# Kernel tuning notes

Measured on AMD Instinct MI355X. Metric: run time of the kernel, lower is better.

The kernel has to match this reference:

```python
import jax, jax.numpy as jnp
import numpy as np

D = 768
H = 16
DH = D // H  # 48
SCALE = 1.0 / np.sqrt(DH).astype(np.float32)
EPS = 1e-3  # keras LayerNormalization default epsilon
NEG = -1e9


def setup_inputs() -> dict:
    key = jax.random.key(0)
    ks = jax.random.split(key, 10)
    B, S = 4, 2048
    q = jax.random.normal(ks[0], (B, S, D), dtype=jnp.float32)
    k = jax.random.normal(ks[1], (B, S, D), dtype=jnp.float32)
    v = jax.random.normal(ks[2], (B, S, D), dtype=jnp.float32)
    # Dense projection params (glorot-ish scale)
    w_std = 1.0 / np.sqrt(D)
    Wq = jax.random.normal(ks[3], (D, D), dtype=jnp.float32) * w_std
    Wk = jax.random.normal(ks[4], (D, D), dtype=jnp.float32) * w_std
    Wv = jax.random.normal(ks[5], (D, D), dtype=jnp.float32) * w_std
    bq = jnp.zeros((D,), jnp.float32)
    bk = jnp.zeros((D,), jnp.float32)
    bv = jnp.zeros((D,), jnp.float32)
    gamma = jnp.ones((D,), jnp.float32)
    beta = jnp.zeros((D,), jnp.float32)
    return {"q": q, "k": k, "v": v, "Wq": Wq, "bq": bq, "Wk": Wk, "bk": bk,
            "Wv": Wv, "bv": bv, "gamma": gamma, "beta": beta}


def reference(q, k, v, Wq, bq, Wk, bk, Wv, bv, gamma, beta):
    use_causal = True  # exercise the causal-mask path
    B, S, _ = q.shape
    # Projections, then split into heads (tf.split on last axis == reshape)
    Q = (q @ Wq + bq).reshape(B, S, H, DH)
    K = (k @ Wk + bk).reshape(B, S, H, DH)
    V = (v @ Wv + bv).reshape(B, S, H, DH)
    # scores: [B, H, Sq, Sk]
    scores = jnp.einsum('bqhd,bkhd->bhqk', Q, K) * SCALE
    if use_causal:
        qi = jnp.arange(S)[:, None]
        ki = jnp.arange(S)[None, :]
        mask = jnp.where(qi >= ki, 0.0, NEG).astype(scores.dtype)
        scores = scores + mask
    attn = jax.nn.softmax(scores, axis=-1)
    out = jnp.einsum('bhqk,bkhd->bqhd', attn, V).reshape(B, S, D)
    # LayerNorm over last dim
    mu = jnp.mean(out, axis=-1, keepdims=True)
    var = jnp.mean(jnp.square(out - mu), axis=-1, keepdims=True)
    return (out - mu) * jax.lax.rsqrt(var + EPS) * gamma + beta
```

## Files before the change

kernel.cpp:

```cpp
#include <hip/hip_runtime.h>
#include <hip/hip_bf16.h>


#define DMODEL 768
#define NHEAD  16
#define DHEAD  48
#define SEQ    2048
#define NBATCH 4
#define NROWS  (NBATCH * SEQ)
#define QSCALE (0.14433756729740643f * 1.4426950408889634f)

typedef __bf16 bf16x8 __attribute__((ext_vector_type(8)));
typedef float  f32x4  __attribute__((ext_vector_type(4)));

#define GLDS16(g, l) __builtin_amdgcn_global_load_lds(                         \
    (const __attribute__((address_space(1))) unsigned int*)(g),                \
    (__attribute__((address_space(3))) unsigned int*)(l), 16, 0, 0)

__global__ __launch_bounds__(256) void transpose_w(
    const float* __restrict__ Wq,
    const float* __restrict__ Wk,
    const float* __restrict__ Wv,
    __hip_bfloat16* __restrict__ Wt)
{
    __shared__ __hip_bfloat16 tile[32][33];
    int bid = blockIdx.x;
    int mat = bid / 576;
    int t   = bid - mat * 576;
    int tr  = t / 24, tc = t - (t / 24) * 24;
    const float* W = (mat == 0) ? Wq : (mat == 1) ? Wk : Wv;
    __hip_bfloat16* O = Wt + (size_t)mat * DMODEL * DMODEL;
    int tx = threadIdx.x & 31, ty = threadIdx.x >> 5;
#pragma unroll
    for (int i = 0; i < 32; i += 8)
        tile[ty + i][tx] = __float2bfloat16(W[(size_t)(tr * 32 + ty + i) * DMODEL + tc * 32 + tx]);
    __syncthreads();
#pragma unroll
    for (int i = 0; i < 32; i += 8)
        O[(size_t)(tc * 32 + ty + i) * DMODEL + tr * 32 + tx] = tile[tx][ty + i];
}

__global__ __launch_bounds__(256) void qkv_proj(
    const float* __restrict__ xq,
    const float* __restrict__ xk,
    const float* __restrict__ xv,
    const __hip_bfloat16* __restrict__ Wt,
    const float* __restrict__ bq,
    const float* __restrict__ bk,
    const float* __restrict__ bv,
    __hip_bfloat16* __restrict__ Qr,
    __hip_bfloat16* __restrict__ Kr,
    __hip_bfloat16* __restrict__ Vt)
{
    __shared__ __hip_bfloat16 As[128 * 32];
    __shared__ __hip_bfloat16 Bs[128 * 32];

    int bid = blockIdx.x;
    int mat = bid / 384;
    int t   = bid - mat * 384;
    int mt  = t / 6, nt = t - (t / 6) * 6;
    int m0  = mt * 128, n0 = nt * 128;

    const float* X          = (mat == 0) ? xq : (mat == 1) ? xk : xv;
    const __hip_bfloat16* W = Wt + (size_t)mat * DMODEL * DMODEL;
    const float* bias       = (mat == 0) ? bq : (mat == 1) ? bk : bv;

    int tid  = threadIdx.x;
    int w    = tid >> 6, lane = tid & 63;
    int l16  = lane & 15, quad = lane >> 4;
    int wm   = w >> 1, wn = w & 1;

    int rowA = tid >> 2;
    int offA = (tid & 3) * 8;

    const float* xb0 = X + (size_t)(m0 + rowA) * DMODEL + offA;
    const float* xb1 = X + (size_t)(m0 + 64 + rowA) * DMODEL + offA;
    const __hip_bfloat16* wb0 = W + (size_t)(n0 + rowA) * DMODEL + offA;
    const __hip_bfloat16* wb1 = W + (size_t)(n0 + 64 + rowA) * DMODEL + offA;

    f32x4 acc[4][4] = {};

    for (int k0 = 0; k0 < DMODEL; k0 += 32) {
        __syncthreads();
        GLDS16(wb0 + k0, &Bs[tid * 8]);
        GLDS16(wb1 + k0, &Bs[2048 + tid * 8]);
        {
            float4 f0 = *(const float4*)(xb0 + k0);
            float4 f1 = *(const float4*)(xb0 + k0 + 4);
            float4 g0 = *(const float4*)(xb1 + k0);
            float4 g1 = *(const float4*)(xb1 + k0 + 4);
            *(bf16x8*)&As[tid * 8] =
                (bf16x8){ (__bf16)f0.x, (__bf16)f0.y, (__bf16)f0.z, (__bf16)f0.w,
                          (__bf16)f1.x, (__bf16)f1.y, (__bf16)f1.z, (__bf16)f1.w };
            *(bf16x8*)&As[2048 + tid * 8] =
                (bf16x8){ (__bf16)g0.x, (__bf16)g0.y, (__bf16)g0.z, (__bf16)g0.w,
                          (__bf16)g1.x, (__bf16)g1.y, (__bf16)g1.z, (__bf16)g1.w };
        }
        __syncthreads();

        bf16x8 a[4], b[4];
#pragma unroll
        for (int i = 0; i < 4; ++i)
            a[i] = *(const bf16x8*)&As[(wm * 64 + i * 16 + l16) * 32 + quad * 8];
#pragma unroll
        for (int j = 0; j < 4; ++j)
            b[j] = *(const bf16x8*)&Bs[(wn * 64 + j * 16 + l16) * 32 + quad * 8];
#pragma unroll
        for (int i = 0; i < 4; ++i)
#pragma unroll
            for (int j = 0; j < 4; ++j)
                acc[i][j] = __builtin_amdgcn_mfma_f32_16x16x32_bf16(a[i], b[j], acc[i][j], 0, 0, 0);
    }

#pragma unroll
    for (int j = 0; j < 4; ++j) {
        int col = n0 + wn * 64 + j * 16 + l16;
        float bc = bias[col];
        if (mat == 0) {
#pragma unroll
            for (int i = 0; i < 4; ++i) {
                int row0 = m0 + wm * 64 + i * 16 + quad * 4;
#pragma unroll
                for (int r = 0; r < 4; ++r)
                    Qr[(size_t)(row0 + r) * DMODEL + col] =
                        __float2bfloat16((acc[i][j][r] + bc) * QSCALE);
            }
        } else if (mat == 1) {
#pragma unroll
            for (int i = 0; i < 4; ++i) {
                int row0 = m0 + wm * 64 + i * 16 + quad * 4;
#pragma unroll
                for (int r = 0; r < 4; ++r)
                    Kr[(size_t)(row0 + r) * DMODEL + col] =
                        __float2bfloat16(acc[i][j][r] + bc);
            }
        } else {
            int h = col / 48, dh = col - h * 48;
#pragma unroll
            for (int i = 0; i < 4; ++i) {
                int row0 = m0 + wm * 64 + i * 16 + quad * 4;
                int bb = row0 >> 11, s0 = row0 & 2047;
                ushort4 pk;
                union { __hip_bfloat16 b; unsigned short u; } cv;
                cv.b = __float2bfloat16(acc[i][j][0] + bc); pk.x = cv.u;
                cv.b = __float2bfloat16(acc[i][j][1] + bc); pk.y = cv.u;
                cv.b = __float2bfloat16(acc[i][j][2] + bc); pk.z = cv.u;
                cv.b = __float2bfloat16(acc[i][j][3] + bc); pk.w = cv.u;
                *(ushort4*)(Vt + ((size_t)(bb * NHEAD + h) * DHEAD + dh) * SEQ + s0) = pk;
            }
        }
    }
}

__global__ __launch_bounds__(256) void attn(
    const __hip_bfloat16* __restrict__ Qr,
    const __hip_bfloat16* __restrict__ Kr,
    const __hip_bfloat16* __restrict__ Vt,
    __hip_bfloat16* __restrict__ Ao)
{
    __shared__ __hip_bfloat16 Ks[2][64][72];
    __shared__ __hip_bfloat16 Vs[2][64][72];
    __shared__ __hip_bfloat16 Ps[4][16][72];

    int tid  = threadIdx.x;
    int w    = tid >> 6, lane = tid & 63;
    int l16  = lane & 15, quad = lane >> 4;
    int bh   = blockIdx.x & 63;
    int qt   = 31 - (blockIdx.x >> 6);
    int q0   = qt * 64;
    int b    = bh >> 4, h = bh & 15;
    size_t rowbase = (size_t)b * SEQ;

    const __hip_bfloat16* Qp = Qr + rowbase * DMODEL + h * DHEAD;
    const __hip_bfloat16* Kp = Kr + rowbase * DMODEL + h * DHEAD;
    const __hip_bfloat16* Vp = Vt + (size_t)bh * DHEAD * SEQ;

    for (int idx = tid; idx < 1024; idx += 256) {
        int buf = idx >> 9, r = (idx >> 3) & 63, c = idx & 7;
        ((unsigned int*)&Ks[buf][r][48])[c] = 0u;
    }
    for (int idx = tid; idx < 2 * 16 * 36; idx += 256) {
        int buf = idx / 576, rem = idx - buf * 576;
        int r = 48 + rem / 36, c = rem - (rem / 36) * 36;
        ((unsigned int*)&Vs[buf][r][0])[c] = (r == 48) ? 0x3F803F80u : 0u;
    }

    int qrow = q0 + w * 16 + l16;
    bf16x8 aQ0 = *(const bf16x8*)(Qp + (size_t)qrow * DMODEL + quad * 8);
    bf16x8 aQ1 = {};
    if (quad < 2) aQ1 = *(const bf16x8*)(Qp + (size_t)qrow * DMODEL + 32 + quad * 8);

    int rK = tid >> 2, oK = (tid & 3) * 12;
    int dV = tid >> 3, oV = (tid & 7) * 8;

    uint2 kr0, kr1, kr2; uint4 vr0, vr1;

#define ATTN_LOAD(kt_) {                                                        \
        int k0_ = (kt_) * 64;                                                   \
        const __hip_bfloat16* kb_ = Kp + (size_t)(k0_ + rK) * DMODEL + oK;      \
        kr0 = *(const uint2*)(kb_);                                             \
        kr1 = *(const uint2*)(kb_ + 4);                                         \
        kr2 = *(const uint2*)(kb_ + 8);                                         \
        vr0 = *(const uint4*)(Vp + (size_t)dV * SEQ + k0_ + oV);                \
        if (tid < 128) vr1 = *(const uint4*)(Vp + (size_t)(32 + dV) * SEQ + k0_ + oV); }

#define ATTN_STORE(buf_) {                                                      \
        __hip_bfloat16* kd_ = &Ks[buf_][rK][oK];                                \
        *(uint2*)(kd_)     = kr0;                                               \
        *(uint2*)(kd_ + 4) = kr1;                                               \
        *(uint2*)(kd_ + 8) = kr2;                                               \
        *(uint4*)&Vs[buf_][dV][oV] = vr0;                                       \
        if (tid < 128) *(uint4*)&Vs[buf_][32 + dV][oV] = vr1; }

    f32x4 O0 = {}, O1 = {}, O2 = {}, O3 = {};

    ATTN_LOAD(0);
    ATTN_STORE(0);
    if (qt >= 1) ATTN_LOAD(1);
    __syncthreads();

    for (int kt = 0; kt <= qt; ++kt) {
        int buf = kt & 1;
        if (kt + 1 <= qt) ATTN_STORE(buf ^ 1);
        if (kt + 2 <= qt) ATTN_LOAD(kt + 2);

        f32x4 s[4];
#pragma unroll
        for (int t = 0; t < 4; ++t) {
            bf16x8 bK0 = *(const bf16x8*)&Ks[buf][l16 + 16 * t][quad * 8];
            bf16x8 bK1 = *(const bf16x8*)&Ks[buf][l16 + 16 * t][32 + quad * 8];
            f32x4 z = {};
            z    = __builtin_amdgcn_mfma_f32_16x16x32_bf16(aQ0, bK0, z, 0, 0, 0);
            s[t] = __builtin_amdgcn_mfma_f32_16x16x32_bf16(aQ1, bK1, z, 0, 0, 0);
        }

        if (kt == qt) {
            int rowi = w * 16 + quad * 4;
#pragma unroll
            for (int t = 0; t < 4; ++t) {
                int colp = t * 16 + l16;
#pragma unroll
                for (int r = 0; r < 4; ++r)
                    if (colp > rowi + r) s[t][r] = -1e30f;
            }
        }

#pragma unroll
        for (int t = 0; t < 4; ++t)
#pragma unroll
            for (int r = 0; r < 4; ++r)
                Ps[w][quad * 4 + r][t * 16 + l16] = __float2bfloat16(exp2f(s[t][r]));

        bf16x8 aP0 = *(const bf16x8*)&Ps[w][l16][quad * 8];
        bf16x8 aP1 = *(const bf16x8*)&Ps[w][l16][32 + quad * 8];
#pragma unroll
        for (int dt = 0; dt < 4; ++dt) {
            bf16x8 b0 = *(const bf16x8*)&Vs[buf][dt * 16 + l16][quad * 8];
            bf16x8 b1 = *(const bf16x8*)&Vs[buf][dt * 16 + l16][32 + quad * 8];
            f32x4* Od = (dt == 0) ? &O0 : (dt == 1) ? &O1 : (dt == 2) ? &O2 : &O3;
            *Od = __builtin_amdgcn_mfma_f32_16x16x32_bf16(aP0, b0, *Od, 0, 0, 0);
            *Od = __builtin_amdgcn_mfma_f32_16x16x32_bf16(aP1, b1, *Od, 0, 0, 0);
        }

        __syncthreads();
    }

    size_t outb = (rowbase + q0 + w * 16 + quad * 4) * DMODEL + h * DHEAD + l16;
#pragma unroll
    for (int r = 0; r < 4; ++r) {
        float lsum = __shfl(O3[r], lane & 48, 64);
        float linv = 1.f / lsum;
        Ao[outb + (size_t)r * DMODEL + 0]  = __float2bfloat16(O0[r] * linv);
        Ao[outb + (size_t)r * DMODEL + 16] = __float2bfloat16(O1[r] * linv);
        Ao[outb + (size_t)r * DMODEL + 32] = __float2bfloat16(O2[r] * linv);
    }
#undef ATTN_LOAD
#undef ATTN_STORE
}

__global__ __launch_bounds__(192) void lnorm(
    const __hip_bfloat16* __restrict__ Ao,
    const float* __restrict__ gamma,
    const float* __restrict__ beta,
    float* __restrict__ out)
{
    __shared__ float rs_[3], rq_[3];
    int row = blockIdx.x;
    int t   = threadIdx.x;
    size_t base = (size_t)row * DMODEL + t * 4;

    ushort4 u = *(const ushort4*)(Ao + base);
    float x0, x1, x2, x3;
    { unsigned int v = (unsigned int)u.x << 16; __builtin_memcpy(&x0, &v, 4); }
    { unsigned int v = (unsigned int)u.y << 16; __builtin_memcpy(&x1, &v, 4); }
    { unsigned int v = (unsigned int)u.z << 16; __builtin_memcpy(&x2, &v, 4); }
    { unsigned int v = (unsigned int)u.w << 16; __builtin_memcpy(&x3, &v, 4); }

    float s = x0 + x1 + x2 + x3;
    float q = x0 * x0 + x1 * x1 + x2 * x2 + x3 * x3;
#pragma unroll
    for (int m = 32; m >= 1; m >>= 1) {
        s += __shfl_xor(s, m, 64);
        q += __shfl_xor(q, m, 64);
    }
    int wv = t >> 6;
    if ((t & 63) == 0) { rs_[wv] = s; rq_[wv] = q; }
    __syncthreads();
    float ts = rs_[0] + rs_[1] + rs_[2];
    float tq = rq_[0] + rq_[1] + rq_[2];
    float mu  = ts * (1.f / 768.f);
    float var = tq * (1.f / 768.f) - mu * mu;
    float rstd = rsqrtf(var + 1e-3f);

    float4 g  = *(const float4*)(gamma + t * 4);
    float4 be = *(const float4*)(beta + t * 4);
    float4 o;
    o.x = (x0 - mu) * rstd * g.x + be.x;
    o.y = (x1 - mu) * rstd * g.y + be.y;
    o.z = (x2 - mu) * rstd * g.z + be.z;
    o.w = (x3 - mu) * rstd * g.w + be.w;
    *(float4*)(out + base) = o;
}

extern "C" void kernel_launch(void* const* d_in, const int* in_sizes, int n_in,
                              void* d_out, int out_size, void* d_ws, size_t ws_size,
                              hipStream_t stream) {
    const float* q     = (const float*)d_in[0];
    const float* k     = (const float*)d_in[1];
    const float* v     = (const float*)d_in[2];
    const float* Wq    = (const float*)d_in[3];
    const float* bq    = (const float*)d_in[4];
    const float* Wk    = (const float*)d_in[5];
    const float* bk    = (const float*)d_in[6];
    const float* Wv    = (const float*)d_in[7];
    const float* bv    = (const float*)d_in[8];
    const float* gamma = (const float*)d_in[9];
    const float* beta  = (const float*)d_in[10];

    char* basep = (char*)d_ws;
    __hip_bfloat16* Wt = (__hip_bfloat16*)basep;
    __hip_bfloat16* Qr = (__hip_bfloat16*)(basep + 3538944);
    __hip_bfloat16* Kr = Qr + (size_t)NROWS * DMODEL;
    __hip_bfloat16* Vt = Kr + (size_t)NROWS * DMODEL;
    __hip_bfloat16* Ao = Vt + (size_t)NROWS * DMODEL;
    float* out = (float*)d_out;

    hipLaunchKernelGGL(transpose_w, dim3(1728), dim3(256), 0, stream, Wq, Wk, Wv, Wt);
    hipLaunchKernelGGL(qkv_proj, dim3(1152), dim3(256), 0, stream,
                       q, k, v, Wt, bq, bk, bv, Qr, Kr, Vt);
    hipLaunchKernelGGL(attn, dim3(2048), dim3(256), 0, stream, Qr, Kr, Vt, Ao);
    hipLaunchKernelGGL(lnorm, dim3(8192), dim3(192), 0, stream, Ao, gamma, beta, out);
}
```

Baseline: 276.8 us.

## Enlarge attention query tile to 128 and remap projection blocks across XCDs

The attention kernel now processes 128 query rows per block, 32 per wave, so each K/V tile loaded into shared memory is reused by twice as many queries and the grid halves. The row sum is accumulated in registers from the exponentiated scores, which replaces the old ones-row trick in V and drops the fourth PV MFMA. Causal skipping now happens per 16-row subtile. The QKV projection block index is remapped so that blocks sharing the same X row tile land on the same XCD for L2 reuse. The cost is higher register and LDS use per block and fewer blocks to balance the causal workload.

Measured after the change: 272.3 us. No clear change (-1.6%).

```diff
diff --git a/kernel.cpp b/kernel.cpp
--- a/kernel.cpp
+++ b/kernel.cpp
@@ -55,11 +55,13 @@
     __shared__ __hip_bfloat16 As[128 * 32];
     __shared__ __hip_bfloat16 Bs[128 * 32];
 
-    int bid = blockIdx.x;
-    int mat = bid / 384;
-    int t   = bid - mat * 384;
-    int mt  = t / 6, nt = t - (t / 6) * 6;
-    int m0  = mt * 128, n0 = nt * 128;
+    int xcd  = blockIdx.x & 7;
+    int s    = blockIdx.x >> 3;
+    int nt   = s % 6;
+    int pair = (s / 6) * 8 + xcd;
+    int mat  = pair >> 6;
+    int mt   = pair & 63;
+    int m0   = mt * 128, n0 = nt * 128;
 
     const float* X          = (mat == 0) ? xq : (mat == 1) ? xk : xv;
     const __hip_bfloat16* W = Wt + (size_t)mat * DMODEL * DMODEL;
@@ -159,15 +161,15 @@
     __hip_bfloat16* __restrict__ Ao)
 {
     __shared__ __hip_bfloat16 Ks[2][64][72];
-    __shared__ __hip_bfloat16 Vs[2][64][72];
-    __shared__ __hip_bfloat16 Ps[4][16][72];
+    __shared__ __hip_bfloat16 Vs[2][48][72];
+    __shared__ __hip_bfloat16 Ps[4][32][72];
 
     int tid  = threadIdx.x;
     int w    = tid >> 6, lane = tid & 63;
     int l16  = lane & 15, quad = lane >> 4;
     int bh   = blockIdx.x & 63;
-    int qt   = 31 - (blockIdx.x >> 6);
-    int q0   = qt * 64;
+    int qt   = 15 - (blockIdx.x >> 6);
+    int q0   = qt * 128;
     int b    = bh >> 4, h = bh & 15;
     size_t rowbase = (size_t)b * SEQ;
 
@@ -179,16 +181,16 @@
         int buf = idx >> 9, r = (idx >> 3) & 63, c = idx & 7;
         ((unsigned int*)&Ks[buf][r][48])[c] = 0u;
     }
-    for (int idx = tid; idx < 2 * 16 * 36; idx += 256) {
-        int buf = idx / 576, rem = idx - buf * 576;
-        int r = 48 + rem / 36, c = rem - (rem / 36) * 36;
-        ((unsigned int*)&Vs[buf][r][0])[c] = (r == 48) ? 0x3F803F80u : 0u;
-    }
-
-    int qrow = q0 + w * 16 + l16;
-    bf16x8 aQ0 = *(const bf16x8*)(Qp + (size_t)qrow * DMODEL + quad * 8);
-    bf16x8 aQ1 = {};
-    if (quad < 2) aQ1 = *(const bf16x8*)(Qp + (size_t)qrow * DMODEL + 32 + quad * 8);
+
+    bf16x8 bQ0[2], bQ1[2];
+#pragma unroll
+    for (int i = 0; i < 2; ++i) {
+        int qrow = q0 + w * 32 + i * 16 + l16;
+        bQ0[i] = *(const bf16x8*)(Qp + (size_t)qrow * DMODEL + quad * 8);
+        bQ1[i] = (bf16x8){};
+        if (quad < 2)
+            bQ1[i] = *(const bf16x8*)(Qp + (size_t)qrow * DMODEL + 32 + quad * 8);
+    }
 
     int rK = tid >> 2, oK = (tid & 3) * 12;
     int dV = tid >> 3, oV = (tid & 7) * 8;
@@ -212,67 +214,105 @@
         *(uint4*)&Vs[buf_][dV][oV] = vr0;                                       \
         if (tid < 128) *(uint4*)&Vs[buf_][32 + dV][oV] = vr1; }
 
-    f32x4 O0 = {}, O1 = {}, O2 = {}, O3 = {};
-
+    f32x4 O[2][3] = {};
+    float lsum[2] = {0.f, 0.f};
+
+    int ktmax = 2 * qt + 1;
     ATTN_LOAD(0);
     ATTN_STORE(0);
-    if (qt >= 1) ATTN_LOAD(1);
+    if (ktmax >= 1) ATTN_LOAD(1);
     __syncthreads();
 
-    for (int kt = 0; kt <= qt; ++kt) {
+    for (int kt = 0; kt <= ktmax; ++kt) {
         int buf = kt & 1;
-        if (kt + 1 <= qt) ATTN_STORE(buf ^ 1);
-        if (kt + 2 <= qt) ATTN_LOAD(kt + 2);
-
-        f32x4 s[4];
+        int k0  = kt * 64;
+        if (kt + 1 <= ktmax) ATTN_STORE(buf ^ 1);
+        if (kt + 2 <= ktmax) ATTN_LOAD(kt + 2);
+
+        bf16x8 aK0[4], aK1[4];
 #pragma unroll
         for (int t = 0; t < 4; ++t) {
-            bf16x8 bK0 = *(const bf16x8*)&Ks[buf][l16 + 16 * t][quad * 8];
-            bf16x8 bK1 = *(const bf16x8*)&Ks[buf][l16 + 16 * t][32 + quad * 8];
-            f32x4 z = {};
-            z    = __builtin_amdgcn_mfma_f32_16x16x32_bf16(aQ0, bK0, z, 0, 0, 0);
-            s[t] = __builtin_amdgcn_mfma_f32_16x16x32_bf16(aQ1, bK1, z, 0, 0, 0);
-        }
-
-        if (kt == qt) {
-            int rowi = w * 16 + quad * 4;
+            aK0[t] = *(const bf16x8*)&Ks[buf][16 * t + l16][quad * 8];
+            aK1[t] = *(const bf16x8*)&Ks[buf][16 * t + l16][32 + quad * 8];
+        }
+
+#pragma unroll
+        for (int i = 0; i < 2; ++i) {
+            int qbase = q0 + w * 32 + i * 16;
+            if (k0 > qbase + 15) continue;
+
+            f32x4 s[4];
 #pragma unroll
             for (int t = 0; t < 4; ++t) {
-                int colp = t * 16 + l16;
-#pragma unroll
-                for (int r = 0; r < 4; ++r)
-                    if (colp > rowi + r) s[t][r] = -1e30f;
-            }
-        }
-
-#pragma unroll
-        for (int t = 0; t < 4; ++t)
-#pragma unroll
-            for (int r = 0; r < 4; ++r)
-                Ps[w][quad * 4 + r][t * 16 + l16] = __float2bfloat16(exp2f(s[t][r]));
-
-        bf16x8 aP0 = *(const bf16x8*)&Ps[w][l16][quad * 8];
-        bf16x8 aP1 = *(const bf16x8*)&Ps[w][l16][32 + quad * 8];
-#pragma unroll
-        for (int dt = 0; dt < 4; ++dt) {
-            bf16x8 b0 = *(const bf16x8*)&Vs[buf][dt * 16 + l16][quad * 8];
-            bf16x8 b1 = *(const bf16x8*)&Vs[buf][dt * 16 + l16][32 + quad * 8];
-            f32x4* Od = (dt == 0) ? &O0 : (dt == 1) ? &O1 : (dt == 2) ? &O2 : &O3;
-            *Od = __builtin_amdgcn_mfma_f32_16x16x32_bf16(aP0, b0, *Od, 0, 0, 0);
-            *Od = __builtin_amdgcn_mfma_f32_16x16x32_bf16(aP1, b1, *Od, 0, 0, 0);
+                f32x4 z = {};
+                z    = __builtin_amdgcn_mfma_f32_16x16x32_bf16(aK0[t], bQ0[i], z, 0, 0, 0);
+                s[t] = __builtin_amdgcn_mfma_f32_16x16x32_bf16(aK1[t], bQ1[i], z, 0, 0, 0);
+            }
+
+            if (k0 + 63 > qbase) {
+                int qg = qbase + l16;
+#pragma unroll
+                for (int t = 0; t < 4; ++t) {
+                    int kg = k0 + 16 * t + quad * 4;
+#pragma unroll
+                    for (int r = 0; r < 4; ++r)
+                        if (kg + r > qg) s[t][r] = -1e30f;
+                }
+            }
+
+            float ls = 0.f;
+#pragma unroll
+            for (int t = 0; t < 4; ++t) {
+                float p0 = exp2f(s[t][0]), p1 = exp2f(s[t][1]);
+                float p2 = exp2f(s[t][2]), p3 = exp2f(s[t][3]);
+                ls += (p0 + p1) + (p2 + p3);
+                union { __bf16 hv[4]; uint2 u2; } pk;
+                pk.hv[0] = (__bf16)p0; pk.hv[1] = (__bf16)p1;
+                pk.hv[2] = (__bf16)p2; pk.hv[3] = (__bf16)p3;
+                *(uint2*)&Ps[w][i * 16 + l16][16 * t + quad * 4] = pk.u2;
+            }
+            lsum[i] += ls;
+        }
+
+        bf16x8 bV0[3], bV1[3];
+#pragma unroll
+        for (int dt = 0; dt < 3; ++dt) {
+            bV0[dt] = *(const bf16x8*)&Vs[buf][dt * 16 + l16][quad * 8];
+            bV1[dt] = *(const bf16x8*)&Vs[buf][dt * 16 + l16][32 + quad * 8];
+        }
+
+#pragma unroll
+        for (int i = 0; i < 2; ++i) {
+            int qbase = q0 + w * 32 + i * 16;
+            if (k0 > qbase + 15) continue;
+            bf16x8 aP0 = *(const bf16x8*)&Ps[w][i * 16 + l16][quad * 8];
+            bf16x8 aP1 = *(const bf16x8*)&Ps[w][i * 16 + l16][32 + quad * 8];
+#pragma unroll
+            for (int dt = 0; dt < 3; ++dt) {
+                O[i][dt] = __builtin_amdgcn_mfma_f32_16x16x32_bf16(aP0, bV0[dt], O[i][dt], 0, 0, 0);
+                O[i][dt] = __builtin_amdgcn_mfma_f32_16x16x32_bf16(aP1, bV1[dt], O[i][dt], 0, 0, 0);
+            }
         }
 
         __syncthreads();
     }
 
-    size_t outb = (rowbase + q0 + w * 16 + quad * 4) * DMODEL + h * DHEAD + l16;
-#pragma unroll
-    for (int r = 0; r < 4; ++r) {
-        float lsum = __shfl(O3[r], lane & 48, 64);
-        float linv = 1.f / lsum;
-        Ao[outb + (size_t)r * DMODEL + 0]  = __float2bfloat16(O0[r] * linv);
-        Ao[outb + (size_t)r * DMODEL + 16] = __float2bfloat16(O1[r] * linv);
-        Ao[outb + (size_t)r * DMODEL + 32] = __float2bfloat16(O2[r] * linv);
+#pragma unroll
+    for (int i = 0; i < 2; ++i) {
+        lsum[i] += __shfl_xor(lsum[i], 16, 64);
+        lsum[i] += __shfl_xor(lsum[i], 32, 64);
+    }
+
+#pragma unroll
+    for (int i = 0; i < 2; ++i) {
+#pragma unroll
+        for (int r = 0; r < 4; ++r) {
+            float linv = 1.f / __shfl(lsum[i], quad * 4 + r, 64);
+            size_t g = (rowbase + q0 + w * 32 + i * 16 + quad * 4 + r) * DMODEL + h * DHEAD + l16;
+            Ao[g + 0]  = __float2bfloat16(O[i][0][r] * linv);
+            Ao[g + 16] = __float2bfloat16(O[i][1][r] * linv);
+            Ao[g + 32] = __float2bfloat16(O[i][2][r] * linv);
+        }
     }
 #undef ATTN_LOAD
 #undef ATTN_STORE
@@ -348,6 +388,6 @@
     hipLaunchKernelGGL(transpose_w, dim3(1728), dim3(256), 0, stream, Wq, Wk, Wv, Wt);
     hipLaunchKernelGGL(qkv_proj, dim3(1152), dim3(256), 0, stream,
                        q, k, v, Wt, bq, bk, bv, Qr, Kr, Vt);
-    hipLaunchKernelGGL(attn, dim3(2048), dim3(256), 0, stream, Qr, Kr, Vt, Ao);
+    hipLaunchKernelGGL(attn, dim3(1024), dim3(256), 0, stream, Qr, Kr, Vt, Ao);
     hipLaunchKernelGGL(lnorm, dim3(8192), dim3(192), 0, stream, Ao, gamma, beta, out);
 }
```
